# Performance work log

Hardware: AMD Instinct MI355X
Metric: run time of the kernel (lower is better)

Reference implementation:

```python
import jax, jax.numpy as jnp
import numpy as np

# Static feature-pyramid shapes (stride 8/16/32 of a 512x512 image)
SPATIAL_SHAPES = ((64, 64), (32, 32), (16, 16))
SEQ = sum(h * w for h, w in SPATIAL_SHAPES)  # 5376
B, D, NH, NL, NP = 4, 256, 8, 3, 4
DH = D // NH  # 32


def _reference_points():
    # normalized pixel centers per level, valid_ratios == 1
    refs = []
    for (h, w) in SPATIAL_SHAPES:
        ry = (jnp.arange(h, dtype=jnp.float32) + 0.5) / h
        rx = (jnp.arange(w, dtype=jnp.float32) + 0.5) / w
        yy, xx = jnp.meshgrid(ry, rx, indexing='ij')
        refs.append(jnp.stack([xx.reshape(-1), yy.reshape(-1)], -1))  # [h*w, 2]
    ref = jnp.concatenate(refs, 0)  # [S, 2]
    return jnp.broadcast_to(ref[None, :, None, :], (B, SEQ, NL, 2))


def setup_inputs() -> dict:
    key = jax.random.key(0)
    ks = jax.random.split(key, 8)
    s = 0.02
    return {
        'hidden_states': jax.random.normal(ks[0], (B, SEQ, D), jnp.float32),
        'position_embeddings': jax.random.normal(ks[1], (B, SEQ, D), jnp.float32),
        'reference_points': _reference_points(),
        'Wv': jax.random.normal(ks[2], (D, D), jnp.float32) * s,
        'bv': jnp.zeros((D,), jnp.float32),
        'Wo': jax.random.normal(ks[3], (D, NH * NL * NP * 2), jnp.float32) * s,
        'bo': jax.random.normal(ks[4], (NH * NL * NP * 2,), jnp.float32) * 0.1,
        'Wa': jax.random.normal(ks[5], (D, NH * NL * NP), jnp.float32) * s,
        'ba': jnp.zeros((NH * NL * NP,), jnp.float32),
        'Wout': jax.random.normal(ks[6], (D, D), jnp.float32) * s,
        'bout': jnp.zeros((D,), jnp.float32),
    }


def _bilinear_sample(img, gx, gy):
    # img: [N, C, H, W]; gx, gy: [N, Q, P] in [-1, 1]
    # grid_sample(mode='bilinear', padding_mode='zeros', align_corners=False)
    N, C, H, W = img.shape
    x = (gx + 1.0) * (W * 0.5) - 0.5
    y = (gy + 1.0) * (H * 0.5) - 0.5
    x0 = jnp.floor(x)
    y0 = jnp.floor(y)
    wx, wy = x - x0, y - y0
    flat = img.reshape(N, C, H * W)
    out = jnp.zeros((N, C) + gx.shape[1:], img.dtype)
    for xi, wxi in ((x0, 1.0 - wx), (x0 + 1.0, wx)):
        for yi, wyi in ((y0, 1.0 - wy), (y0 + 1.0, wy)):
            valid = (xi >= 0) & (xi < W) & (yi >= 0) & (yi < H)
            xc = jnp.clip(xi, 0, W - 1).astype(jnp.int32)
            yc = jnp.clip(yi, 0, H - 1).astype(jnp.int32)
            idx = (yc * W + xc).reshape(N, 1, -1)  # [N,1,Q*P]
            v = jnp.take_along_axis(flat, idx, axis=2).reshape(N, C, *gx.shape[1:])
            out = out + v * (wxi * wyi * valid.astype(img.dtype))[:, None]
    return out  # [N, C, Q, P]


def reference(hidden_states, position_embeddings, reference_points,
              Wv, bv, Wo, bo, Wa, ba, Wout, bout):
    hs = hidden_states + position_embeddings  # queries carry pos embed
    value = hidden_states @ Wv + bv           # value from raw encoder states
    value = value.reshape(B, SEQ, NH, DH)

    off = (hs @ Wo + bo).reshape(B, SEQ, NH, NL, NP, 2)
    attn = jax.nn.softmax((hs @ Wa + ba).reshape(B, SEQ, NH, NL * NP), -1)
    attn = attn.reshape(B, SEQ, NH, NL, NP)

    # offset normalizer: [W_l, H_l] per level
    norm = jnp.array([[w, h] for (h, w) in SPATIAL_SHAPES], jnp.float32)
    loc = reference_points[:, :, None, :, None, :] + off / norm[None, None, None, :, None, :]
    grid = 2.0 * loc - 1.0  # [B, Q, H, L, P, 2]

    sampled = []
    start = 0
    for lvl, (h, w) in enumerate(SPATIAL_SHAPES):
        v_l = value[:, start:start + h * w]  # [B, h*w, H, d]
        start += h * w
        v_l = v_l.transpose(0, 2, 3, 1).reshape(B * NH, DH, h, w)
        g_l = grid[:, :, :, lvl].transpose(0, 2, 1, 3, 4).reshape(B * NH, SEQ, NP, 2)
        sampled.append(_bilinear_sample(v_l, g_l[..., 0], g_l[..., 1]))  # [B*H,d,Q,P]
    sampled = jnp.stack(sampled, -2).reshape(B * NH, DH, SEQ, NL * NP)

    aw = attn.transpose(0, 2, 1, 3, 4).reshape(B * NH, 1, SEQ, NL * NP)
    out = (sampled * aw).sum(-1)                   # [B*H, d, Q]
    out = out.reshape(B, NH * DH, SEQ).transpose(0, 2, 1)  # [B, Q, D]
    out = out @ Wout + bout
    return out, attn
```

## Files before the change

kernel.cpp:

```cpp
#include <hip/hip_runtime.h>
#include <hip/hip_bf16.h>
#include <math.h>

#define BB 4
#define SEQ 5376
#define DD 256
#define NH 8
#define NL 3
#define NP 4
#define DH 32
#define MTOT (BB * SEQ)

typedef __attribute__((ext_vector_type(8))) short bf16x8;
typedef __attribute__((ext_vector_type(4))) float f32x4;

__device__ __forceinline__ ushort f2b(float f) {
    __hip_bfloat16 h = __float2bfloat16(f);
    return *reinterpret_cast<ushort*>(&h);
}

__global__ __launch_bounds__(256) void prep_all(
    const float* __restrict__ hidden, const float* __restrict__ pos,
    const float* __restrict__ Wv, const float* __restrict__ Wo,
    const float* __restrict__ Wa, const float* __restrict__ Wout,
    const float* __restrict__ bo, const float* __restrict__ ba,
    ushort4* __restrict__ hb, ushort4* __restrict__ hsb,
    ushort* __restrict__ Wt, float* __restrict__ bcomb, int n4) {
    int bid = blockIdx.x;
    int tid = threadIdx.x;
    if (bid <= 800) {
        if (bid == 800) {
            for (int i = tid; i < 288; i += 256)
                bcomb[i] = (i < 192) ? bo[i] : ba[i - 192];
            return;
        }
        int row = bid;
        const float* src;
        int N, n;
        if (row < 256)      { src = Wv;   N = 256; n = row; }
        else if (row < 448) { src = Wo;   N = 192; n = row - 256; }
        else if (row < 544) { src = Wa;   N = 96;  n = row - 448; }
        else                { src = Wout; N = 256; n = row - 544; }
        float v = src[(size_t)tid * N + n];
        Wt[(size_t)row * 256 + tid] = f2b(v);
        return;
    }
    const float4* h4 = (const float4*)hidden;
    const float4* p4 = (const float4*)pos;
    int i = (bid - 801) * 256 + tid;
    int stride = (gridDim.x - 801) * 256;
    for (; i < n4; i += stride) {
        float4 a = h4[i], b = p4[i];
        ushort4 ua, us;
        ua.x = f2b(a.x); ua.y = f2b(a.y); ua.z = f2b(a.z); ua.w = f2b(a.w);
        us.x = f2b(a.x + b.x); us.y = f2b(a.y + b.y);
        us.z = f2b(a.z + b.z); us.w = f2b(a.w + b.w);
        hb[i] = ua;
        hsb[i] = us;
    }
}

template<bool OBF>
__global__ __launch_bounds__(256) void gemm_mfma(
    const ushort* __restrict__ A, const ushort* __restrict__ Wt,
    const float* __restrict__ bias, void* __restrict__ Cout,
    int M, int N, int K) {
    const int BM = 128, BN = 128, BK = 64, PK = 72;
    __shared__ ushort As[BM][PK];
    __shared__ ushort Bs[BN][PK];
    int bm = blockIdx.y * BM;
    int bn = blockIdx.x * BN;
    int tid = threadIdx.x;
    int lane = tid & 63;
    int wid = tid >> 6;
    int wr = wid >> 1, wc = wid & 1;
    int lr = lane & 15;
    int kg = lane >> 4;

    f32x4 acc[4][4] = {};

    for (int k0 = 0; k0 < K; k0 += BK) {
        #pragma unroll
        for (int c = 0; c < 4; c++) {
            int e = tid + 256 * c;
            int row = e >> 3, q = e & 7;
            const ushort* src = A + (size_t)(bm + row) * K + k0 + 8 * q;
            *(bf16x8*)&As[row][8 * q] = *(const bf16x8*)src;
        }
        #pragma unroll
        for (int c = 0; c < 4; c++) {
            int e = tid + 256 * c;
            int row = e >> 3, q = e & 7;
            int gn = bn + row;
            bf16x8 v = {0, 0, 0, 0, 0, 0, 0, 0};
            if (gn < N) v = *(const bf16x8*)(Wt + (size_t)gn * K + k0 + 8 * q);
            *(bf16x8*)&Bs[row][8 * q] = v;
        }
        __syncthreads();
        #pragma unroll
        for (int ks = 0; ks < 2; ks++) {
            bf16x8 af[4], bfr[4];
            #pragma unroll
            for (int mf = 0; mf < 4; mf++)
                af[mf] = *(bf16x8*)&As[wr * 64 + mf * 16 + lr][ks * 32 + kg * 8];
            #pragma unroll
            for (int nf = 0; nf < 4; nf++)
                bfr[nf] = *(bf16x8*)&Bs[wc * 64 + nf * 16 + lr][ks * 32 + kg * 8];
            #pragma unroll
            for (int mf = 0; mf < 4; mf++)
                #pragma unroll
                for (int nf = 0; nf < 4; nf++)
                    acc[mf][nf] = __builtin_amdgcn_mfma_f32_16x16x32_bf16(
                        af[mf], bfr[nf], acc[mf][nf], 0, 0, 0);
        }
        __syncthreads();
    }

    #pragma unroll
    for (int nf = 0; nf < 4; nf++) {
        int gc = bn + wc * 64 + nf * 16 + lr;
        if (gc >= N) continue;
        float bv = bias[gc];
        #pragma unroll
        for (int mf = 0; mf < 4; mf++) {
            int gr0 = bm + wr * 64 + mf * 16 + kg * 4;
            #pragma unroll
            for (int r = 0; r < 4; r++) {
                float v = acc[mf][nf][r] + bv;
                if constexpr (OBF)
                    ((ushort*)Cout)[(size_t)(gr0 + r) * N + gc] = f2b(v);
                else
                    ((float*)Cout)[(size_t)(gr0 + r) * N + gc] = v;
            }
        }
    }
}

struct Acc8 {
    float a0, a1, a2, a3, a4, a5, a6, a7;
};

__device__ __forceinline__ void fma8(Acc8& acc, float wt, uint4 u) {
    acc.a0 = fmaf(wt, __uint_as_float(u.x << 16), acc.a0);
    acc.a1 = fmaf(wt, __uint_as_float(u.x & 0xffff0000u), acc.a1);
    acc.a2 = fmaf(wt, __uint_as_float(u.y << 16), acc.a2);
    acc.a3 = fmaf(wt, __uint_as_float(u.y & 0xffff0000u), acc.a3);
    acc.a4 = fmaf(wt, __uint_as_float(u.z << 16), acc.a4);
    acc.a5 = fmaf(wt, __uint_as_float(u.z & 0xffff0000u), acc.a5);
    acc.a6 = fmaf(wt, __uint_as_float(u.w << 16), acc.a6);
    acc.a7 = fmaf(wt, __uint_as_float(u.w & 0xffff0000u), acc.a7);
}

__global__ __launch_bounds__(64) void msda_sample_v8(
    const ushort* __restrict__ value, const float* __restrict__ comb,
    const float* __restrict__ refp, float* __restrict__ attn_out,
    ushort* __restrict__ out) {
    __shared__ int4   s_idx[2][8][13];
    __shared__ float4 s_w[2][8][13];
    int tid = threadIdx.x;
    int bq0 = blockIdx.x * 2;

    #pragma unroll
    for (int it = 0; it < 4; it++) {
        int t = tid + it * 64;
        int lp = t & 15;
        int qh = t >> 4;
        int q = qh >> 3, h = qh & 7;
        int bq = bq0 + q;
        bool active = lp < 12;
        const float* crow = comb + (size_t)bq * 288;
        float logit = active ? crow[192 + h * 12 + lp] : -INFINITY;
        float m = logit;
        m = fmaxf(m, __shfl_xor(m, 1, 16));
        m = fmaxf(m, __shfl_xor(m, 2, 16));
        m = fmaxf(m, __shfl_xor(m, 4, 16));
        m = fmaxf(m, __shfl_xor(m, 8, 16));
        float e = active ? expf(logit - m) : 0.f;
        float s = e;
        s += __shfl_xor(s, 1, 16);
        s += __shfl_xor(s, 2, 16);
        s += __shfl_xor(s, 4, 16);
        s += __shfl_xor(s, 8, 16);
        float aw = e / s;
        if (active) {
            attn_out[(size_t)bq * 96 + h * 12 + lp] = aw;
            int l = lp >> 2;
            int b = bq / SEQ;
            int Wl = 64 >> l;
            float fW = (float)Wl;
            float rx = refp[(size_t)bq * 6 + 2 * l];
            float ry = refp[(size_t)bq * 6 + 2 * l + 1];
            float ox = crow[h * 24 + lp * 2];
            float oy = crow[h * 24 + lp * 2 + 1];
            float x = rx * fW + ox - 0.5f;
            float y = ry * fW + oy - 0.5f;
            float x0f = floorf(x), y0f = floorf(y);
            float wx = x - x0f, wy = y - y0f;
            int x0 = (int)x0f, y0 = (int)y0f;
            int x1 = x0 + 1, y1 = y0 + 1;
            float vx0 = (x0 >= 0 && x0 < Wl) ? 1.f : 0.f;
            float vx1 = (x1 >= 0 && x1 < Wl) ? 1.f : 0.f;
            float vy0 = (y0 >= 0 && y0 < Wl) ? 1.f : 0.f;
            float vy1 = (y1 >= 0 && y1 < Wl) ? 1.f : 0.f;
            int xc0 = min(max(x0, 0), Wl - 1);
            int xc1 = min(max(x1, 0), Wl - 1);
            int yc0 = min(max(y0, 0), Wl - 1);
            int yc1 = min(max(y1, 0), Wl - 1);
            int st = (l == 0) ? 0 : ((l == 1) ? 4096 : 5120);
            int rowbase = b * SEQ + st;
            s_idx[q][h][lp] = make_int4((rowbase + yc0 * Wl + xc0) << 8,
                                        (rowbase + yc0 * Wl + xc1) << 8,
                                        (rowbase + yc1 * Wl + xc0) << 8,
                                        (rowbase + yc1 * Wl + xc1) << 8);
            s_w[q][h][lp] = make_float4(aw * (1.f - wx) * (1.f - wy) * vx0 * vy0,
                                        aw * wx * (1.f - wy) * vx1 * vy0,
                                        aw * (1.f - wx) * wy * vx0 * vy1,
                                        aw * wx * wy * vx1 * vy1);
        }
    }
    __syncthreads();

    int q = tid >> 5;
    int lane5 = tid & 31;
    int h = lane5 >> 2, d8 = lane5 & 3;
    int bq = bq0 + q;
    int ch0 = h * 32 + d8 * 8;
    const ushort* vb = value + ch0;

    Acc8 acc = {0.f, 0.f, 0.f, 0.f, 0.f, 0.f, 0.f, 0.f};
    #pragma unroll
    for (int lp = 0; lp < 12; lp++) {
        int4 ii = s_idx[q][h][lp];
        float4 ww = s_w[q][h][lp];
        uint4 u0 = *(const uint4*)(vb + ii.x);
        uint4 u1 = *(const uint4*)(vb + ii.y);
        uint4 u2 = *(const uint4*)(vb + ii.z);
        uint4 u3 = *(const uint4*)(vb + ii.w);
        fma8(acc, ww.x, u0);
        fma8(acc, ww.y, u1);
        fma8(acc, ww.z, u2);
        fma8(acc, ww.w, u3);
    }

    bf16x8 o;
    o[0] = (short)f2b(acc.a0); o[1] = (short)f2b(acc.a1);
    o[2] = (short)f2b(acc.a2); o[3] = (short)f2b(acc.a3);
    o[4] = (short)f2b(acc.a4); o[5] = (short)f2b(acc.a5);
    o[6] = (short)f2b(acc.a6); o[7] = (short)f2b(acc.a7);
    *(bf16x8*)(out + (size_t)bq * 256 + ch0) = o;
}

extern "C" void kernel_launch(void* const* d_in, const int* in_sizes, int n_in,
                              void* d_out, int out_size, void* d_ws, size_t ws_size,
                              hipStream_t stream) {
    const float* hidden = (const float*)d_in[0];
    const float* pos    = (const float*)d_in[1];
    const float* refp   = (const float*)d_in[2];
    const float* Wv     = (const float*)d_in[3];
    const float* bv     = (const float*)d_in[4];
    const float* Wo     = (const float*)d_in[5];
    const float* bo     = (const float*)d_in[6];
    const float* Wa     = (const float*)d_in[7];
    const float* ba     = (const float*)d_in[8];
    const float* Wout   = (const float*)d_in[9];
    const float* bout   = (const float*)d_in[10];

    float* out      = (float*)d_out;
    float* attn_out = out + (size_t)BB * SEQ * DD;

    const size_t BSD = (size_t)BB * SEQ * DD;
    char* w = (char*)d_ws;
    ushort* value_bf = (ushort*)w;  w += BSD * 2;
    float*  comb     = (float*)w;   w += (size_t)MTOT * 288 * 4;
    ushort* sampb    = (ushort*)w;  w += BSD * 2;
    ushort* hb       = (ushort*)w;  w += BSD * 2;
    ushort* hsb      = (ushort*)w;  w += BSD * 2;
    ushort* Wt       = (ushort*)w;  w += (size_t)800 * 256 * 2;
    float*  bcomb    = (float*)w;

    {
        int n4 = (int)(BSD / 4);
        prep_all<<<801 + 2048, 256, 0, stream>>>(hidden, pos, Wv, Wo, Wa, Wout,
                                                 bo, ba, (ushort4*)hb, (ushort4*)hsb,
                                                 Wt, bcomb, n4);
    }

    const ushort* Wv_t    = Wt;
    const ushort* Wcomb_t = Wt + (size_t)256 * 256;
    const ushort* Wout_t  = Wt + (size_t)544 * 256;

    {
        dim3 grid(DD / 128, MTOT / 128);
        gemm_mfma<true><<<grid, 256, 0, stream>>>(hb, Wv_t, bv, value_bf, MTOT, DD, DD);
    }
    {
        dim3 grid(3, MTOT / 128);
        gemm_mfma<false><<<grid, 256, 0, stream>>>(hsb, Wcomb_t, bcomb, comb, MTOT, 288, DD);
    }
    {
        msda_sample_v8<<<MTOT / 2, 64, 0, stream>>>(value_bf, comb, refp,
                                                    attn_out, sampb);
    }
    {
        dim3 grid(DD / 128, MTOT / 128);
        gemm_mfma<false><<<grid, 256, 0, stream>>>(sampb, Wout_t, bout, out, MTOT, DD, DD);
    }
}
```

Baseline: 94.98 us.

## Use direct global-to-LDS loads with XOR swizzle in GEMM; widen sampler blocks

The MFMA GEMM now loads its A and B tiles with global_load_lds 16-byte transfers straight into shared memory. This skips the trip through registers and replaces the padded tile layout with an XOR-swizzled one to avoid LDS bank conflicts on fragment reads. The bounds guard on the weight rows is gone, so the 288-column projection's last tile reads past the end of its weights into the following Wout rows; those output columns are already discarded in the epilogue. Separately, the deformable sampling kernel now runs 128-thread blocks that handle four queries instead of two, which reduces block count and scheduling overhead per query.

```diff
diff --git a/kernel.cpp b/kernel.cpp
--- a/kernel.cpp
+++ b/kernel.cpp
@@ -13,6 +13,10 @@
 
 typedef __attribute__((ext_vector_type(8))) short bf16x8;
 typedef __attribute__((ext_vector_type(4))) float f32x4;
+
+#define GLD_LDS16(src, dst) __builtin_amdgcn_global_load_lds( \
+    (const __attribute__((address_space(1))) void*)(src),     \
+    (__attribute__((address_space(3))) void*)(dst), 16, 0, 0)
 
 __device__ __forceinline__ ushort f2b(float f) {
     __hip_bfloat16 h = __float2bfloat16(f);
@@ -65,11 +69,11 @@
     const ushort* __restrict__ A, const ushort* __restrict__ Wt,
     const float* __restrict__ bias, void* __restrict__ Cout,
     int M, int N, int K) {
-    const int BM = 128, BN = 128, BK = 64, PK = 72;
-    __shared__ ushort As[BM][PK];
-    __shared__ ushort Bs[BN][PK];
-    int bm = blockIdx.y * BM;
-    int bn = blockIdx.x * BN;
+    const int BK = 64;
+    __shared__ ushort As[128 * 64];
+    __shared__ ushort Bs[128 * 64];
+    int bm = blockIdx.y * 128;
+    int bn = blockIdx.x * 128;
     int tid = threadIdx.x;
     int lane = tid & 63;
     int wid = tid >> 6;
@@ -83,29 +87,28 @@
         #pragma unroll
         for (int c = 0; c < 4; c++) {
             int e = tid + 256 * c;
-            int row = e >> 3, q = e & 7;
-            const ushort* src = A + (size_t)(bm + row) * K + k0 + 8 * q;
-            *(bf16x8*)&As[row][8 * q] = *(const bf16x8*)src;
-        }
-        #pragma unroll
-        for (int c = 0; c < 4; c++) {
-            int e = tid + 256 * c;
-            int row = e >> 3, q = e & 7;
-            int gn = bn + row;
-            bf16x8 v = {0, 0, 0, 0, 0, 0, 0, 0};
-            if (gn < N) v = *(const bf16x8*)(Wt + (size_t)gn * K + k0 + 8 * q);
-            *(bf16x8*)&Bs[row][8 * q] = v;
+            int row = e >> 3;
+            int ch = e & 7;
+            int gch = ch ^ (row & 7);
+            GLD_LDS16(A + (size_t)(bm + row) * K + k0 + 8 * gch, &As[e * 8]);
+            GLD_LDS16(Wt + (size_t)(bn + row) * K + k0 + 8 * gch, &Bs[e * 8]);
         }
         __syncthreads();
         #pragma unroll
         for (int ks = 0; ks < 2; ks++) {
             bf16x8 af[4], bfr[4];
             #pragma unroll
-            for (int mf = 0; mf < 4; mf++)
-                af[mf] = *(bf16x8*)&As[wr * 64 + mf * 16 + lr][ks * 32 + kg * 8];
+            for (int mf = 0; mf < 4; mf++) {
+                int R = wr * 64 + mf * 16 + lr;
+                int sc = (ks * 4 + kg) ^ (R & 7);
+                af[mf] = *(bf16x8*)&As[R * 64 + sc * 8];
+            }
             #pragma unroll
-            for (int nf = 0; nf < 4; nf++)
-                bfr[nf] = *(bf16x8*)&Bs[wc * 64 + nf * 16 + lr][ks * 32 + kg * 8];
+            for (int nf = 0; nf < 4; nf++) {
+                int R = wc * 64 + nf * 16 + lr;
+                int sc = (ks * 4 + kg) ^ (R & 7);
+                bfr[nf] = *(bf16x8*)&Bs[R * 64 + sc * 8];
+            }
             #pragma unroll
             for (int mf = 0; mf < 4; mf++)
                 #pragma unroll
@@ -151,18 +154,18 @@
     acc.a7 = fmaf(wt, __uint_as_float(u.w & 0xffff0000u), acc.a7);
 }
 
-__global__ __launch_bounds__(64) void msda_sample_v8(
+__global__ __launch_bounds__(128) void msda_sample_v7(
     const ushort* __restrict__ value, const float* __restrict__ comb,
     const float* __restrict__ refp, float* __restrict__ attn_out,
     ushort* __restrict__ out) {
-    __shared__ int4   s_idx[2][8][13];
-    __shared__ float4 s_w[2][8][13];
+    __shared__ int4   s_idx[4][8][13];
+    __shared__ float4 s_w[4][8][13];
     int tid = threadIdx.x;
-    int bq0 = blockIdx.x * 2;
+    int bq0 = blockIdx.x * 4;
 
     #pragma unroll
     for (int it = 0; it < 4; it++) {
-        int t = tid + it * 64;
+        int t = tid + it * 128;
         int lp = t & 15;
         int qh = t >> 4;
         int q = qh >> 3, h = qh & 7;
@@ -220,9 +223,11 @@
     }
     __syncthreads();
 
-    int q = tid >> 5;
-    int lane5 = tid & 31;
+    int wave = tid >> 6, lane = tid & 63;
+    int q2 = lane >> 5;
+    int lane5 = lane & 31;
     int h = lane5 >> 2, d8 = lane5 & 3;
+    int q = wave * 2 + q2;
     int bq = bq0 + q;
     int ch0 = h * 32 + d8 * 8;
     const ushort* vb = value + ch0;
@@ -298,8 +303,8 @@
         gemm_mfma<false><<<grid, 256, 0, stream>>>(hsb, Wcomb_t, bcomb, comb, MTOT, 288, DD);
     }
     {
-        msda_sample_v8<<<MTOT / 2, 64, 0, stream>>>(value_bf, comb, refp,
-                                                    attn_out, sampb);
+        msda_sample_v7<<<MTOT / 4, 128, 0, stream>>>(value_bf, comb, refp,
+                                                     attn_out, sampb);
     }
     {
         dim3 grid(DD / 128, MTOT / 128);
```

After: 83.43 us. 12.2% less time.
